# Kernel optimization log

Hardware: AMD Instinct MI355X
Metric: run time of the kernel (lower is better)

Reference implementation:

```python
import jax, jax.numpy as jnp
import numpy as np

N_NODES = 100000


def gcn_conv(x, src, dst, W, b, n):
    # PyG GCNConv: add self-loops (weight 1), symmetric deg^-1/2 normalization,
    # linear transform, scatter-add to targets, then bias.
    loop = jnp.arange(n, dtype=src.dtype)
    s = jnp.concatenate([src, loop])
    d = jnp.concatenate([dst, loop])
    w = jnp.ones(s.shape[0], dtype=x.dtype)
    deg = jax.ops.segment_sum(w, d, num_segments=n)
    dis = jnp.where(deg > 0, jax.lax.rsqrt(deg), 0.0)
    norm = dis[s] * w * dis[d]                      # [E+N]
    h = x @ W                                       # [N, out]
    msg = h[s] * norm[:, None]                      # [E+N, out]
    out = jax.ops.segment_sum(msg, d, num_segments=n)
    return out + b


def setup_inputs() -> dict:
    key = jax.random.key(0)
    ks = jax.random.split(key, 8)
    num_node_types, emb_dim, hidden_dim, out_dim = 1000, 128, 128, 64
    n, e = N_NODES, 1600000
    x_node_types = jax.random.randint(ks[0], (n,), 0, num_node_types, dtype=jnp.int64 if jax.config.jax_enable_x64 else jnp.int32)
    edge_index = jax.random.randint(ks[1], (2, e), 0, n, dtype=x_node_types.dtype)
    emb = jax.random.normal(ks[2], (num_node_types, emb_dim), dtype=jnp.float32)
    W1 = jax.random.normal(ks[3], (emb_dim, hidden_dim), dtype=jnp.float32) / np.sqrt(emb_dim)
    b1 = jnp.zeros((hidden_dim,), dtype=jnp.float32)
    W2 = jax.random.normal(ks[4], (hidden_dim, out_dim), dtype=jnp.float32) / np.sqrt(hidden_dim)
    b2 = jnp.zeros((out_dim,), dtype=jnp.float32)
    return {"x_node_types": x_node_types, "edge_index": edge_index,
            "emb": emb, "W1": W1, "b1": b1, "W2": W2, "b2": b2}


def reference(x_node_types, edge_index, emb, W1, b1, W2, b2):
    n = N_NODES
    src, dst = edge_index[0], edge_index[1]
    x = emb[x_node_types]                           # embedding lookup [N, emb_dim]
    x = jax.nn.relu(gcn_conv(x, src, dst, W1, b1, n))
    # dropout p=0.5 is identity in eval mode (training=False)
    x = gcn_conv(x, src, dst, W2, b2, n)
    return x
```

## Files before the change

### kernel.cpp

```cpp
#include <hip/hip_runtime.h>
#include <hip/hip_bf16.h>


#define D1 128
#define D2 64
#define BSH 9
#define BW  512
#define BMAX 256
#define TILE 2048
#define SMASK 0x1FFFF

typedef __attribute__((ext_vector_type(8))) short short8v;
typedef __attribute__((ext_vector_type(8))) unsigned short ushort8v;
typedef __attribute__((ext_vector_type(4))) float f32x4;

__device__ __forceinline__ short bf16_hi(float x) {
    return (short)(__float_as_uint(x) >> 16);
}
__device__ __forceinline__ float hi_f(float x) {
    return __uint_as_float(__float_as_uint(x) & 0xFFFF0000u);
}
__device__ __forceinline__ short bf16_rne(float x) {
    unsigned u = __float_as_uint(x);
    return (short)((u + 0x7FFFu + ((u >> 16) & 1u)) >> 16);
}
__device__ __forceinline__ float bf16_f(unsigned short u) {
    return __uint_as_float((unsigned)u << 16);
}

__global__ __launch_bounds__(256) void bhist_k(const int* __restrict__ dst,
                                               int* __restrict__ bcnt, int e) {
    __shared__ int h[BMAX];
    if (threadIdx.x < BMAX) h[threadIdx.x] = 0;
    __syncthreads();
    int stride = gridDim.x * blockDim.x;
    for (int t = blockIdx.x * blockDim.x + threadIdx.x; t < e; t += stride)
        atomicAdd(&h[dst[t] >> BSH], 1);
    __syncthreads();
    if (threadIdx.x < BMAX && h[threadIdx.x])
        atomicAdd(&bcnt[threadIdx.x], h[threadIdx.x]);
}

__global__ void bscan_k(const int* __restrict__ bcnt, int* __restrict__ bbase,
                        int* __restrict__ bcur, int nb) {
    __shared__ int tmp[BMAX];
    int tid = threadIdx.x;
    int v = (tid < nb) ? bcnt[tid] : 0;
    tmp[tid] = v;
    __syncthreads();
    for (int s = 1; s < BMAX; s <<= 1) {
        int a = (tid >= s) ? tmp[tid - s] : 0;
        __syncthreads();
        tmp[tid] += a;
        __syncthreads();
    }
    if (tid < nb) { int ex = tmp[tid] - v; bbase[tid] = ex; bcur[tid] = ex; }
}

__global__ __launch_bounds__(256) void bpart_k(const int* __restrict__ src,
                                               const int* __restrict__ dst,
                                               int* __restrict__ bcur,
                                               unsigned* __restrict__ ebuf, int e) {
    __shared__ int hist[BMAX];
    __shared__ int chunk[BMAX];
    __shared__ int lcur[BMAX];
    int tid = threadIdx.x;
    int base = blockIdx.x * TILE;
    if (tid < BMAX) { hist[tid] = 0; lcur[tid] = 0; }
    __syncthreads();
    unsigned p8[8];
    int b8[8];
    #pragma unroll
    for (int i = 0; i < 8; ++i) {
        int t = base + i * 256 + tid;
        if (t < e) {
            int s = src[t], d = dst[t];
            b8[i] = d >> BSH;
            p8[i] = (unsigned)s | ((unsigned)(d & (BW - 1)) << 17);
            atomicAdd(&hist[b8[i]], 1);
        } else b8[i] = -1;
    }
    __syncthreads();
    if (tid < BMAX && hist[tid]) chunk[tid] = atomicAdd(&bcur[tid], hist[tid]);
    __syncthreads();
    #pragma unroll
    for (int i = 0; i < 8; ++i) {
        if (b8[i] >= 0) {
            int r = atomicAdd(&lcur[b8[i]], 1);
            ebuf[chunk[b8[i]] + r] = p8[i];
        }
    }
}

__global__ __launch_bounds__(512) void bcsr_count_k(const unsigned* __restrict__ ebuf,
                                                    const int* __restrict__ bbase,
                                                    const int* __restrict__ bcnt,
                                                    int* __restrict__ cnt,
                                                    int* __restrict__ off,
                                                    float* __restrict__ dis, int n) {
    __shared__ int lcnt[BW];
    __shared__ int lsc[BW];
    int b = blockIdx.x;
    int d0 = b << BSH;
    int tid = threadIdx.x;
    lcnt[tid] = 0;
    __syncthreads();
    int ebase = bbase[b], ecnt = bcnt[b];
    for (int t = tid; t < ecnt; t += BW)
        atomicAdd(&lcnt[ebuf[ebase + t] >> 17], 1);
    __syncthreads();
    int v = lcnt[tid];
    lsc[tid] = v;
    __syncthreads();
    for (int s = 1; s < BW; s <<= 1) {
        int a = (tid >= s) ? lsc[tid - s] : 0;
        __syncthreads();
        lsc[tid] += a;
        __syncthreads();
    }
    int node = d0 + tid;
    if (node < n) {
        cnt[node] = v;
        off[node] = ebase + lsc[tid] - v;
        dis[node] = rsqrtf((float)(v + 1));
    }
}

__global__ __launch_bounds__(512) void bcsr_fill_k(const unsigned* __restrict__ ebuf,
                                                   const int* __restrict__ bbase,
                                                   const int* __restrict__ bcnt,
                                                   const int* __restrict__ off,
                                                   const float* __restrict__ dis,
                                                   const int* __restrict__ types,
                                                   int2* __restrict__ csr_p, int n) {
    __shared__ int loff[BW];
    __shared__ float ldis[BW];
    __shared__ int lcur[BW];
    int b = blockIdx.x;
    int d0 = b << BSH;
    int tid = threadIdx.x;
    int node = d0 + tid;
    lcur[tid] = 0;
    if (node < n) { loff[tid] = off[node]; ldis[tid] = dis[node]; }
    __syncthreads();
    int ebase = bbase[b], ecnt = bcnt[b];
    for (int t = tid; t < ecnt; t += BW) {
        unsigned q = ebuf[ebase + t];
        int l = q >> 17;
        int s = q & SMASK;
        int r = atomicAdd(&lcur[l], 1);
        float coef = ldis[l] * dis[s];
        csr_p[loff[l] + r] = make_int2(s | (types[s] << 17), __float_as_int(coef));
    }
}

__global__ void w2prep_k(const float* __restrict__ W2,
                         short* __restrict__ w2h, short* __restrict__ w2l) {
    int t = blockIdx.x * blockDim.x + threadIdx.x;
    if (t >= D1 * D2) return;
    int k = t >> 6, c = t & 63;
    float v = W2[t];
    int ct = c >> 4, kb = k >> 5;
    int l = (((k >> 3) & 3) << 4) | (c & 15);
    int j = k & 7;
    int idx = (((ct << 2) | kb) * 64 + l) * 8 + j;
    w2h[idx] = bf16_hi(v);
    w2l[idx] = bf16_rne(v - hi_f(v));
}

__global__ __launch_bounds__(128) void gemm_emb_k(const float* __restrict__ emb,
                                                  const float* __restrict__ W1,
                                                  unsigned short* __restrict__ embWb,
                                                  int ntypes) {
    __shared__ float w[D1 * D1];
    for (int t = threadIdx.x; t < D1 * D1; t += 128) w[t] = W1[t];
    __syncthreads();
    int j = threadIdx.x;
    for (int r = blockIdx.x; r < ntypes; r += gridDim.x) {
        const float* er = emb + (size_t)r * D1;
        float acc = 0.f;
        #pragma unroll 8
        for (int k = 0; k < D1; ++k) acc = fmaf(er[k], w[k * D1 + j], acc);
        embWb[(size_t)r * D1 + j] = (unsigned short)bf16_rne(acc);
    }
}

__global__ __launch_bounds__(256) void agg1_k(const int* __restrict__ types,
                                              const int2* __restrict__ csr_p,
                                              const int* __restrict__ off,
                                              const int* __restrict__ cnt,
                                              const float* __restrict__ dis,
                                              const unsigned short* __restrict__ embWb,
                                              const float* __restrict__ b1,
                                              float* __restrict__ x1, int n) {
    int gw = (blockIdx.x * blockDim.x + threadIdx.x) >> 6;
    int lane = threadIdx.x & 63;
    int sub = lane >> 4;
    int sl = lane & 15;
    int i = gw * 4 + sub;
    bool ok = i < n;
    int ii = ok ? i : 0;
    float disi = dis[ii];
    int base = off[ii];
    int c = ok ? cnt[ii] : 0;
    const unsigned short* ewb = embWb + (sl << 3);
    float4 a0, a1, a2, a3;
    {
        float cf = disi * disi;
        ushort8v r = *(const ushort8v*)(ewb + (size_t)types[ii] * D1);
        a0.x = bf16_f(r[0]) * cf; a0.y = bf16_f(r[1]) * cf;
        a0.z = bf16_f(r[2]) * cf; a0.w = bf16_f(r[3]) * cf;
        a1.x = bf16_f(r[4]) * cf; a1.y = bf16_f(r[5]) * cf;
        a1.z = bf16_f(r[6]) * cf; a1.w = bf16_f(r[7]) * cf;
    }
    a2 = make_float4(0.f, 0.f, 0.f, 0.f);
    a3 = a2;
    if (c > 0) {
        int cm = c - 1;
        int2 p0 = csr_p[base];
        int2 p1 = csr_p[base + min(1, cm)];
        int2 p2 = csr_p[base + min(2, cm)];
        int2 p3 = csr_p[base + min(3, cm)];
        for (int k = 0; k < c; k += 4) {
            int2 q0 = csr_p[base + min(k + 4, cm)];
            int2 q1 = csr_p[base + min(k + 5, cm)];
            int2 q2 = csr_p[base + min(k + 6, cm)];
            int2 q3 = csr_p[base + min(k + 7, cm)];
            ushort8v r0 = *(const ushort8v*)(ewb + (size_t)(p0.x >> 17) * D1);
            ushort8v r1 = *(const ushort8v*)(ewb + (size_t)(p1.x >> 17) * D1);
            ushort8v r2 = *(const ushort8v*)(ewb + (size_t)(p2.x >> 17) * D1);
            ushort8v r3 = *(const ushort8v*)(ewb + (size_t)(p3.x >> 17) * D1);
            float c0 = __int_as_float(p0.y);
            float c1 = (k + 1 < c) ? __int_as_float(p1.y) : 0.f;
            float c2 = (k + 2 < c) ? __int_as_float(p2.y) : 0.f;
            float c3 = (k + 3 < c) ? __int_as_float(p3.y) : 0.f;
            a0.x = fmaf(bf16_f(r0[0]), c0, a0.x); a0.y = fmaf(bf16_f(r0[1]), c0, a0.y);
            a0.z = fmaf(bf16_f(r0[2]), c0, a0.z); a0.w = fmaf(bf16_f(r0[3]), c0, a0.w);
            a1.x = fmaf(bf16_f(r0[4]), c0, a1.x); a1.y = fmaf(bf16_f(r0[5]), c0, a1.y);
            a1.z = fmaf(bf16_f(r0[6]), c0, a1.z); a1.w = fmaf(bf16_f(r0[7]), c0, a1.w);
            a2.x = fmaf(bf16_f(r1[0]), c1, a2.x); a2.y = fmaf(bf16_f(r1[1]), c1, a2.y);
            a2.z = fmaf(bf16_f(r1[2]), c1, a2.z); a2.w = fmaf(bf16_f(r1[3]), c1, a2.w);
            a3.x = fmaf(bf16_f(r1[4]), c1, a3.x); a3.y = fmaf(bf16_f(r1[5]), c1, a3.y);
            a3.z = fmaf(bf16_f(r1[6]), c1, a3.z); a3.w = fmaf(bf16_f(r1[7]), c1, a3.w);
            a0.x = fmaf(bf16_f(r2[0]), c2, a0.x); a0.y = fmaf(bf16_f(r2[1]), c2, a0.y);
            a0.z = fmaf(bf16_f(r2[2]), c2, a0.z); a0.w = fmaf(bf16_f(r2[3]), c2, a0.w);
            a1.x = fmaf(bf16_f(r2[4]), c2, a1.x); a1.y = fmaf(bf16_f(r2[5]), c2, a1.y);
            a1.z = fmaf(bf16_f(r2[6]), c2, a1.z); a1.w = fmaf(bf16_f(r2[7]), c2, a1.w);
            a2.x = fmaf(bf16_f(r3[0]), c3, a2.x); a2.y = fmaf(bf16_f(r3[1]), c3, a2.y);
            a2.z = fmaf(bf16_f(r3[2]), c3, a2.z); a2.w = fmaf(bf16_f(r3[3]), c3, a2.w);
            a3.x = fmaf(bf16_f(r3[4]), c3, a3.x); a3.y = fmaf(bf16_f(r3[5]), c3, a3.y);
            a3.z = fmaf(bf16_f(r3[6]), c3, a3.z); a3.w = fmaf(bf16_f(r3[7]), c3, a3.w);
            p0 = q0; p1 = q1; p2 = q2; p3 = q3;
        }
    }
    if (ok) {
        float4 f0 = make_float4(a0.x + a2.x, a0.y + a2.y, a0.z + a2.z, a0.w + a2.w);
        float4 f1 = make_float4(a1.x + a3.x, a1.y + a3.y, a1.z + a3.z, a1.w + a3.w);
        float4 bv0 = ((const float4*)b1)[sl * 2];
        float4 bv1 = ((const float4*)b1)[sl * 2 + 1];
        f0.x = fmaxf(f0.x + bv0.x, 0.f); f0.y = fmaxf(f0.y + bv0.y, 0.f);
        f0.z = fmaxf(f0.z + bv0.z, 0.f); f0.w = fmaxf(f0.w + bv0.w, 0.f);
        f1.x = fmaxf(f1.x + bv1.x, 0.f); f1.y = fmaxf(f1.y + bv1.y, 0.f);
        f1.z = fmaxf(f1.z + bv1.z, 0.f); f1.w = fmaxf(f1.w + bv1.w, 0.f);
        ((float4*)(x1 + (size_t)i * D1))[sl * 2] = f0;
        ((float4*)(x1 + (size_t)i * D1))[sl * 2 + 1] = f1;
    }
}

__global__ __launch_bounds__(256) void gemm2_k(const float* __restrict__ x1,
                                               const short* __restrict__ w2h,
                                               const short* __restrict__ w2l,
                                               unsigned short* __restrict__ h2b, int n) {
    int gw = (blockIdx.x * blockDim.x + threadIdx.x) >> 6;
    int lane = threadIdx.x & 63;
    int r0 = gw << 4;
    if (r0 >= n) return;
    int row = r0 + (lane & 15);
    int kq = lane >> 4;
    bool ok = row < n;
    const float* xr = x1 + (size_t)row * D1 + kq * 8;
    short8v ah[4], al[4];
    #pragma unroll
    for (int kb = 0; kb < 4; ++kb) {
        float4 v0, v1;
        if (ok) {
            v0 = *(const float4*)(xr + kb * 32);
            v1 = *(const float4*)(xr + kb * 32 + 4);
        } else {
            v0 = make_float4(0.f, 0.f, 0.f, 0.f);
            v1 = v0;
        }
        float xv[8] = {v0.x, v0.y, v0.z, v0.w, v1.x, v1.y, v1.z, v1.w};
        #pragma unroll
        for (int j = 0; j < 8; ++j) {
            ah[kb][j] = bf16_hi(xv[j]);
            al[kb][j] = bf16_rne(xv[j] - hi_f(xv[j]));
        }
    }
    const short8v* w2hv = (const short8v*)w2h;
    const short8v* w2lv = (const short8v*)w2l;
    #pragma unroll
    for (int ct = 0; ct < 4; ++ct) {
        f32x4 acc = {0.f, 0.f, 0.f, 0.f};
        #pragma unroll
        for (int kb = 0; kb < 4; ++kb) {
            short8v bh = w2hv[(ct * 4 + kb) * 64 + lane];
            short8v bl = w2lv[(ct * 4 + kb) * 64 + lane];
            acc = __builtin_amdgcn_mfma_f32_16x16x32_bf16(ah[kb], bh, acc, 0, 0, 0);
            acc = __builtin_amdgcn_mfma_f32_16x16x32_bf16(al[kb], bh, acc, 0, 0, 0);
            acc = __builtin_amdgcn_mfma_f32_16x16x32_bf16(ah[kb], bl, acc, 0, 0, 0);
        }
        #pragma unroll
        for (int v = 0; v < 4; ++v) {
            int orow = r0 + (lane >> 4) * 4 + v;
            if (orow < n)
                h2b[(size_t)orow * D2 + ct * 16 + (lane & 15)] =
                    (unsigned short)bf16_rne(acc[v]);
        }
    }
}

__global__ __launch_bounds__(256) void agg2_k(const int2* __restrict__ csr_p,
                                              const int* __restrict__ off,
                                              const int* __restrict__ cnt,
                                              const float* __restrict__ dis,
                                              const unsigned short* __restrict__ h2b,
                                              const float* __restrict__ b2,
                                              float* __restrict__ out, int n) {
    int gw = (blockIdx.x * blockDim.x + threadIdx.x) >> 6;
    int lane = threadIdx.x & 63;
    int sub = lane >> 4;
    int sl = lane & 15;
    int i = gw * 4 + sub;
    bool ok = i < n;
    int ii = ok ? i : 0;
    float disi = dis[ii];
    int base = off[ii];
    int c = ok ? cnt[ii] : 0;
    const unsigned short* hb = h2b + (sl << 2);
    float4 a0, a1;
    {
        float cf = disi * disi;
        ushort4 r = *(const ushort4*)(hb + (size_t)ii * D2);
        a0.x = bf16_f(r.x) * cf; a0.y = bf16_f(r.y) * cf;
        a0.z = bf16_f(r.z) * cf; a0.w = bf16_f(r.w) * cf;
    }
    a1 = make_float4(0.f, 0.f, 0.f, 0.f);
    if (c > 0) {
        int cm = c - 1;
        int2 p0 = csr_p[base];
        int2 p1 = csr_p[base + min(1, cm)];
        int2 p2 = csr_p[base + min(2, cm)];
        int2 p3 = csr_p[base + min(3, cm)];
        for (int k = 0; k < c; k += 4) {
            int2 q0 = csr_p[base + min(k + 4, cm)];
            int2 q1 = csr_p[base + min(k + 5, cm)];
            int2 q2 = csr_p[base + min(k + 6, cm)];
            int2 q3 = csr_p[base + min(k + 7, cm)];
            ushort4 r0 = *(const ushort4*)(hb + (size_t)(p0.x & SMASK) * D2);
            ushort4 r1 = *(const ushort4*)(hb + (size_t)(p1.x & SMASK) * D2);
            ushort4 r2 = *(const ushort4*)(hb + (size_t)(p2.x & SMASK) * D2);
            ushort4 r3 = *(const ushort4*)(hb + (size_t)(p3.x & SMASK) * D2);
            float c0 = __int_as_float(p0.y);
            float c1 = (k + 1 < c) ? __int_as_float(p1.y) : 0.f;
            float c2 = (k + 2 < c) ? __int_as_float(p2.y) : 0.f;
            float c3 = (k + 3 < c) ? __int_as_float(p3.y) : 0.f;
            a0.x = fmaf(bf16_f(r0.x), c0, a0.x); a0.y = fmaf(bf16_f(r0.y), c0, a0.y);
            a0.z = fmaf(bf16_f(r0.z), c0, a0.z); a0.w = fmaf(bf16_f(r0.w), c0, a0.w);
            a1.x = fmaf(bf16_f(r1.x), c1, a1.x); a1.y = fmaf(bf16_f(r1.y), c1, a1.y);
            a1.z = fmaf(bf16_f(r1.z), c1, a1.z); a1.w = fmaf(bf16_f(r1.w), c1, a1.w);
            a0.x = fmaf(bf16_f(r2.x), c2, a0.x); a0.y = fmaf(bf16_f(r2.y), c2, a0.y);
            a0.z = fmaf(bf16_f(r2.z), c2, a0.z); a0.w = fmaf(bf16_f(r2.w), c2, a0.w);
            a1.x = fmaf(bf16_f(r3.x), c3, a1.x); a1.y = fmaf(bf16_f(r3.y), c3, a1.y);
            a1.z = fmaf(bf16_f(r3.z), c3, a1.z); a1.w = fmaf(bf16_f(r3.w), c3, a1.w);
            p0 = q0; p1 = q1; p2 = q2; p3 = q3;
        }
    }
    if (ok) {
        float4 bv = ((const float4*)b2)[sl];
        float4 f;
        f.x = a0.x + a1.x + bv.x;
        f.y = a0.y + a1.y + bv.y;
        f.z = a0.z + a1.z + bv.z;
        f.w = a0.w + a1.w + bv.w;
        ((float4*)(out + (size_t)i * D2))[sl] = f;
    }
}

extern "C" void kernel_launch(void* const* d_in, const int* in_sizes, int n_in,
                              void* d_out, int out_size, void* d_ws, size_t ws_size,
                              hipStream_t stream) {
    const int* types = (const int*)d_in[0];
    const int* edges = (const int*)d_in[1];
    const float* emb = (const float*)d_in[2];
    const float* W1  = (const float*)d_in[3];
    const float* b1  = (const float*)d_in[4];
    const float* W2  = (const float*)d_in[5];
    const float* b2  = (const float*)d_in[6];
    float* out = (float*)d_out;

    const int n = in_sizes[0];
    const int e = in_sizes[1] / 2;
    const int ntypes = in_sizes[2] / D1;
    const int* src = edges;
    const int* dst = edges + e;
    const int nb = (n + BW - 1) >> BSH;

    char* p = (char*)d_ws;
    auto alloc = [&](size_t bytes) {
        char* r = p;
        p += (bytes + 255) & ~(size_t)255;
        return r;
    };
    int*      bcnt  = (int*)      alloc(BMAX * 4);
    int*      bbase = (int*)      alloc(BMAX * 4);
    int*      bcur  = (int*)      alloc(BMAX * 4);
    int*      cnt   = (int*)      alloc((size_t)n * 4);
    int*      off   = (int*)      alloc((size_t)n * 4);
    float*    dis   = (float*)    alloc((size_t)n * 4);
    short*    w2h   = (short*)    alloc((size_t)D1 * D2 * 2);
    short*    w2l   = (short*)    alloc((size_t)D1 * D2 * 2);
    unsigned* ebuf  = (unsigned*) alloc((size_t)e * 4);
    int2*     csr_p = (int2*)     alloc((size_t)e * 8);
    unsigned short* embWb = (unsigned short*)alloc((size_t)ntypes * D1 * 2);
    float*    x1    = (float*)    alloc((size_t)n * D1 * 4);
    unsigned short* h2b = (unsigned short*)alloc((size_t)n * D2 * 2);
    (void)ws_size;

    hipMemsetAsync(bcnt, 0, BMAX * 4, stream);

    bhist_k<<<512, 256, 0, stream>>>(dst, bcnt, e);
    bscan_k<<<1, BMAX, 0, stream>>>(bcnt, bbase, bcur, nb);
    bpart_k<<<(e + TILE - 1) / TILE, 256, 0, stream>>>(src, dst, bcur, ebuf, e);
    bcsr_count_k<<<nb, BW, 0, stream>>>(ebuf, bbase, bcnt, cnt, off, dis, n);
    bcsr_fill_k<<<nb, BW, 0, stream>>>(ebuf, bbase, bcnt, off, dis, types, csr_p, n);
    w2prep_k<<<(D1 * D2 + 255) / 256, 256, 0, stream>>>(W2, w2h, w2l);

    gemm_emb_k<<<256, 128, 0, stream>>>(emb, W1, embWb, ntypes);
    int ngrid = (n + 15) / 16;
    agg1_k<<<ngrid, 256, 0, stream>>>(types, csr_p, off, cnt, dis, embWb, b1, x1, n);

    int ngw = (n + 15) / 16;
    gemm2_k<<<(ngw + 3) / 4, 256, 0, stream>>>(x1, w2h, w2l, h2b, n);
    agg2_k<<<ngrid, 256, 0, stream>>>(csr_p, off, cnt, dis, h2b, b2, out, n);
}
```

Baseline: 269.2 us.

## Map one wavefront per node in both aggregation kernels instead of four

Both aggregation kernels now give each 64-lane wavefront a single destination node, with each lane holding 2 features (agg1) or 1 feature (agg2), where before 16 lanes shared a node and each lane held 8 or 4 features. This removes the divergence caused by uneven per-node degree inside a wavefront and lowers register pressure. In exchange the grid grows fourfold and every wavefront issues its own CSR index loads. Gathers become narrower 32-bit or 16-bit accesses instead of 128-bit or 64-bit ones, so fewer neighbor loads are in flight per lane.

```diff
diff --git a/kernel.cpp b/kernel.cpp
--- a/kernel.cpp
+++ b/kernel.cpp
@@ -11,7 +11,6 @@
 #define SMASK 0x1FFFF
 
 typedef __attribute__((ext_vector_type(8))) short short8v;
-typedef __attribute__((ext_vector_type(8))) unsigned short ushort8v;
 typedef __attribute__((ext_vector_type(4))) float f32x4;
 
 __device__ __forceinline__ short bf16_hi(float x) {
@@ -26,6 +25,12 @@
 }
 __device__ __forceinline__ float bf16_f(unsigned short u) {
     return __uint_as_float((unsigned)u << 16);
+}
+__device__ __forceinline__ float bf16_lo_f(unsigned r) {
+    return __uint_as_float(r << 16);
+}
+__device__ __forceinline__ float bf16_hi_f(unsigned r) {
+    return __uint_as_float(r & 0xFFFF0000u);
 }
 
 __global__ __launch_bounds__(256) void bhist_k(const int* __restrict__ dst,
@@ -193,28 +198,20 @@
                                               const unsigned short* __restrict__ embWb,
                                               const float* __restrict__ b1,
                                               float* __restrict__ x1, int n) {
-    int gw = (blockIdx.x * blockDim.x + threadIdx.x) >> 6;
+    int i = (blockIdx.x * blockDim.x + threadIdx.x) >> 6;
+    if (i >= n) return;
     int lane = threadIdx.x & 63;
-    int sub = lane >> 4;
-    int sl = lane & 15;
-    int i = gw * 4 + sub;
-    bool ok = i < n;
-    int ii = ok ? i : 0;
-    float disi = dis[ii];
-    int base = off[ii];
-    int c = ok ? cnt[ii] : 0;
-    const unsigned short* ewb = embWb + (sl << 3);
-    float4 a0, a1, a2, a3;
+    float disi = dis[i];
+    int base = off[i], c = cnt[i];
+    const unsigned short* ew = embWb + lane * 2;
+    float2 a0, a1;
     {
         float cf = disi * disi;
-        ushort8v r = *(const ushort8v*)(ewb + (size_t)types[ii] * D1);
-        a0.x = bf16_f(r[0]) * cf; a0.y = bf16_f(r[1]) * cf;
-        a0.z = bf16_f(r[2]) * cf; a0.w = bf16_f(r[3]) * cf;
-        a1.x = bf16_f(r[4]) * cf; a1.y = bf16_f(r[5]) * cf;
-        a1.z = bf16_f(r[6]) * cf; a1.w = bf16_f(r[7]) * cf;
-    }
-    a2 = make_float4(0.f, 0.f, 0.f, 0.f);
-    a3 = a2;
+        unsigned r = *(const unsigned*)(ew + (size_t)types[i] * D1);
+        a0.x = bf16_lo_f(r) * cf;
+        a0.y = bf16_hi_f(r) * cf;
+    }
+    a1.x = 0.f; a1.y = 0.f;
     if (c > 0) {
         int cm = c - 1;
         int2 p0 = csr_p[base];
@@ -226,45 +223,30 @@
             int2 q1 = csr_p[base + min(k + 5, cm)];
             int2 q2 = csr_p[base + min(k + 6, cm)];
             int2 q3 = csr_p[base + min(k + 7, cm)];
-            ushort8v r0 = *(const ushort8v*)(ewb + (size_t)(p0.x >> 17) * D1);
-            ushort8v r1 = *(const ushort8v*)(ewb + (size_t)(p1.x >> 17) * D1);
-            ushort8v r2 = *(const ushort8v*)(ewb + (size_t)(p2.x >> 17) * D1);
-            ushort8v r3 = *(const ushort8v*)(ewb + (size_t)(p3.x >> 17) * D1);
+            unsigned r0 = *(const unsigned*)(ew + (size_t)(p0.x >> 17) * D1);
+            unsigned r1 = *(const unsigned*)(ew + (size_t)(p1.x >> 17) * D1);
+            unsigned r2 = *(const unsigned*)(ew + (size_t)(p2.x >> 17) * D1);
+            unsigned r3 = *(const unsigned*)(ew + (size_t)(p3.x >> 17) * D1);
             float c0 = __int_as_float(p0.y);
             float c1 = (k + 1 < c) ? __int_as_float(p1.y) : 0.f;
             float c2 = (k + 2 < c) ? __int_as_float(p2.y) : 0.f;
             float c3 = (k + 3 < c) ? __int_as_float(p3.y) : 0.f;
-            a0.x = fmaf(bf16_f(r0[0]), c0, a0.x); a0.y = fmaf(bf16_f(r0[1]), c0, a0.y);
-            a0.z = fmaf(bf16_f(r0[2]), c0, a0.z); a0.w = fmaf(bf16_f(r0[3]), c0, a0.w);
-            a1.x = fmaf(bf16_f(r0[4]), c0, a1.x); a1.y = fmaf(bf16_f(r0[5]), c0, a1.y);
-            a1.z = fmaf(bf16_f(r0[6]), c0, a1.z); a1.w = fmaf(bf16_f(r0[7]), c0, a1.w);
-            a2.x = fmaf(bf16_f(r1[0]), c1, a2.x); a2.y = fmaf(bf16_f(r1[1]), c1, a2.y);
-            a2.z = fmaf(bf16_f(r1[2]), c1, a2.z); a2.w = fmaf(bf16_f(r1[3]), c1, a2.w);
-            a3.x = fmaf(bf16_f(r1[4]), c1, a3.x); a3.y = fmaf(bf16_f(r1[5]), c1, a3.y);
-            a3.z = fmaf(bf16_f(r1[6]), c1, a3.z); a3.w = fmaf(bf16_f(r1[7]), c1, a3.w);
-            a0.x = fmaf(bf16_f(r2[0]), c2, a0.x); a0.y = fmaf(bf16_f(r2[1]), c2, a0.y);
-            a0.z = fmaf(bf16_f(r2[2]), c2, a0.z); a0.w = fmaf(bf16_f(r2[3]), c2, a0.w);
-            a1.x = fmaf(bf16_f(r2[4]), c2, a1.x); a1.y = fmaf(bf16_f(r2[5]), c2, a1.y);
-            a1.z = fmaf(bf16_f(r2[6]), c2, a1.z); a1.w = fmaf(bf16_f(r2[7]), c2, a1.w);
-            a2.x = fmaf(bf16_f(r3[0]), c3, a2.x); a2.y = fmaf(bf16_f(r3[1]), c3, a2.y);
-            a2.z = fmaf(bf16_f(r3[2]), c3, a2.z); a2.w = fmaf(bf16_f(r3[3]), c3, a2.w);
-            a3.x = fmaf(bf16_f(r3[4]), c3, a3.x); a3.y = fmaf(bf16_f(r3[5]), c3, a3.y);
-            a3.z = fmaf(bf16_f(r3[6]), c3, a3.z); a3.w = fmaf(bf16_f(r3[7]), c3, a3.w);
+            a0.x = fmaf(bf16_lo_f(r0), c0, a0.x);
+            a0.y = fmaf(bf16_hi_f(r0), c0, a0.y);
+            a1.x = fmaf(bf16_lo_f(r1), c1, a1.x);
+            a1.y = fmaf(bf16_hi_f(r1), c1, a1.y);
+            a0.x = fmaf(bf16_lo_f(r2), c2, a0.x);
+            a0.y = fmaf(bf16_hi_f(r2), c2, a0.y);
+            a1.x = fmaf(bf16_lo_f(r3), c3, a1.x);
+            a1.y = fmaf(bf16_hi_f(r3), c3, a1.y);
             p0 = q0; p1 = q1; p2 = q2; p3 = q3;
         }
     }
-    if (ok) {
-        float4 f0 = make_float4(a0.x + a2.x, a0.y + a2.y, a0.z + a2.z, a0.w + a2.w);
-        float4 f1 = make_float4(a1.x + a3.x, a1.y + a3.y, a1.z + a3.z, a1.w + a3.w);
-        float4 bv0 = ((const float4*)b1)[sl * 2];
-        float4 bv1 = ((const float4*)b1)[sl * 2 + 1];
-        f0.x = fmaxf(f0.x + bv0.x, 0.f); f0.y = fmaxf(f0.y + bv0.y, 0.f);
-        f0.z = fmaxf(f0.z + bv0.z, 0.f); f0.w = fmaxf(f0.w + bv0.w, 0.f);
-        f1.x = fmaxf(f1.x + bv1.x, 0.f); f1.y = fmaxf(f1.y + bv1.y, 0.f);
-        f1.z = fmaxf(f1.z + bv1.z, 0.f); f1.w = fmaxf(f1.w + bv1.w, 0.f);
-        ((float4*)(x1 + (size_t)i * D1))[sl * 2] = f0;
-        ((float4*)(x1 + (size_t)i * D1))[sl * 2 + 1] = f1;
-    }
+    float2 bv = ((const float2*)b1)[lane];
+    float2 f;
+    f.x = fmaxf(a0.x + a1.x + bv.x, 0.f);
+    f.y = fmaxf(a0.y + a1.y + bv.y, 0.f);
+    ((float2*)(x1 + (size_t)i * D1))[lane] = f;
 }
 
 __global__ __launch_bounds__(256) void gemm2_k(const float* __restrict__ x1,
@@ -327,25 +309,17 @@
                                               const unsigned short* __restrict__ h2b,
                                               const float* __restrict__ b2,
                                               float* __restrict__ out, int n) {
-    int gw = (blockIdx.x * blockDim.x + threadIdx.x) >> 6;
+    int i = (blockIdx.x * blockDim.x + threadIdx.x) >> 6;
+    if (i >= n) return;
     int lane = threadIdx.x & 63;
-    int sub = lane >> 4;
-    int sl = lane & 15;
-    int i = gw * 4 + sub;
-    bool ok = i < n;
-    int ii = ok ? i : 0;
-    float disi = dis[ii];
-    int base = off[ii];
-    int c = ok ? cnt[ii] : 0;
-    const unsigned short* hb = h2b + (sl << 2);
-    float4 a0, a1;
+    float disi = dis[i];
+    int base = off[i], c = cnt[i];
+    const unsigned short* hb = h2b + lane;
+    float a0, a1;
     {
-        float cf = disi * disi;
-        ushort4 r = *(const ushort4*)(hb + (size_t)ii * D2);
-        a0.x = bf16_f(r.x) * cf; a0.y = bf16_f(r.y) * cf;
-        a0.z = bf16_f(r.z) * cf; a0.w = bf16_f(r.w) * cf;
-    }
-    a1 = make_float4(0.f, 0.f, 0.f, 0.f);
+        a0 = bf16_f(hb[(size_t)i * D2]) * (disi * disi);
+    }
+    a1 = 0.f;
     if (c > 0) {
         int cm = c - 1;
         int2 p0 = csr_p[base];
@@ -357,34 +331,22 @@
             int2 q1 = csr_p[base + min(k + 5, cm)];
             int2 q2 = csr_p[base + min(k + 6, cm)];
             int2 q3 = csr_p[base + min(k + 7, cm)];
-            ushort4 r0 = *(const ushort4*)(hb + (size_t)(p0.x & SMASK) * D2);
-            ushort4 r1 = *(const ushort4*)(hb + (size_t)(p1.x & SMASK) * D2);
-            ushort4 r2 = *(const ushort4*)(hb + (size_t)(p2.x & SMASK) * D2);
-            ushort4 r3 = *(const ushort4*)(hb + (size_t)(p3.x & SMASK) * D2);
+            unsigned short r0 = hb[(size_t)(p0.x & SMASK) * D2];
+            unsigned short r1 = hb[(size_t)(p1.x & SMASK) * D2];
+            unsigned short r2 = hb[(size_t)(p2.x & SMASK) * D2];
+            unsigned short r3 = hb[(size_t)(p3.x & SMASK) * D2];
             float c0 = __int_as_float(p0.y);
             float c1 = (k + 1 < c) ? __int_as_float(p1.y) : 0.f;
             float c2 = (k + 2 < c) ? __int_as_float(p2.y) : 0.f;
             float c3 = (k + 3 < c) ? __int_as_float(p3.y) : 0.f;
-            a0.x = fmaf(bf16_f(r0.x), c0, a0.x); a0.y = fmaf(bf16_f(r0.y), c0, a0.y);
-            a0.z = fmaf(bf16_f(r0.z), c0, a0.z); a0.w = fmaf(bf16_f(r0.w), c0, a0.w);
-            a1.x = fmaf(bf16_f(r1.x), c1, a1.x); a1.y = fmaf(bf16_f(r1.y), c1, a1.y);
-            a1.z = fmaf(bf16_f(r1.z), c1, a1.z); a1.w = fmaf(bf16_f(r1.w), c1, a1.w);
-            a0.x = fmaf(bf16_f(r2.x), c2, a0.x); a0.y = fmaf(bf16_f(r2.y), c2, a0.y);
-            a0.z = fmaf(bf16_f(r2.z), c2, a0.z); a0.w = fmaf(bf16_f(r2.w), c2, a0.w);
-            a1.x = fmaf(bf16_f(r3.x), c3, a1.x); a1.y = fmaf(bf16_f(r3.y), c3, a1.y);
-            a1.z = fmaf(bf16_f(r3.z), c3, a1.z); a1.w = fmaf(bf16_f(r3.w), c3, a1.w);
+            a0 = fmaf(bf16_f(r0), c0, a0);
+            a1 = fmaf(bf16_f(r1), c1, a1);
+            a0 = fmaf(bf16_f(r2), c2, a0);
+            a1 = fmaf(bf16_f(r3), c3, a1);
             p0 = q0; p1 = q1; p2 = q2; p3 = q3;
         }
     }
-    if (ok) {
-        float4 bv = ((const float4*)b2)[sl];
-        float4 f;
-        f.x = a0.x + a1.x + bv.x;
-        f.y = a0.y + a1.y + bv.y;
-        f.z = a0.z + a1.z + bv.z;
-        f.w = a0.w + a1.w + bv.w;
-        ((float4*)(out + (size_t)i * D2))[sl] = f;
-    }
+    out[(size_t)i * D2 + lane] = a0 + a1 + b2[lane];
 }
 
 extern "C" void kernel_launch(void* const* d_in, const int* in_sizes, int n_in,
@@ -437,7 +399,7 @@
     w2prep_k<<<(D1 * D2 + 255) / 256, 256, 0, stream>>>(W2, w2h, w2l);
 
     gemm_emb_k<<<256, 128, 0, stream>>>(emb, W1, embWb, ntypes);
-    int ngrid = (n + 15) / 16;
+    int ngrid = (n + 3) / 4;
     agg1_k<<<ngrid, 256, 0, stream>>>(types, csr_p, off, cnt, dis, embWb, b1, x1, n);
 
     int ngw = (n + 15) / 16;
```

After: 340.7 us. +26.6%, slower.
